# Performance work log

Measured on AMD Instinct MI355X. Metric: run time of the kernel, lower is better.

The kernel has to match this reference:

```python
import jax, jax.numpy as jnp
import numpy as np

C, E, H, TOPK = 768, 8, 3072, 2
B, T = 2048, 1

def setup_inputs() -> dict:
    key = jax.random.key(0)
    ks = jax.random.split(key, 5)
    proj_std = 0.02 * (2 * 12) ** (-0.5)  # n_layer = 12
    return {
        "x": jax.random.normal(ks[0], (B, T, C), jnp.float32),
        "w_router": 0.02 * jax.random.normal(ks[1], (C, E), jnp.float32),
        "w_c_fc": 0.02 * jax.random.normal(ks[2], (E, C, H), jnp.float32),
        "b_c_fc": jnp.zeros((E, 1, H), jnp.float32),
        "w_gate": 0.02 * jax.random.normal(ks[3], (E, C, H), jnp.float32),
        "b_gate": jnp.zeros((E, 1, H), jnp.float32),
        "w_c_proj": proj_std * jax.random.normal(ks[4], (E, H, C), jnp.float32),
        "b_c_proj": jnp.zeros((E, 1, C), jnp.float32),
        "top_k": TOPK,
    }

def reference(x, w_router, w_c_fc, b_c_fc, w_gate, b_gate, w_c_proj, b_c_proj, top_k):
    Bx, Tx, Cx = x.shape
    n_experts = w_c_fc.shape[0]
    xf = x.reshape(-1, Cx)                      # (N, C), N = B*T
    N = xf.shape[0]
    logits = xf @ w_router                      # (N, E); router has no bias (mlp_bias=False)
    top_k_logits, expert_indices = jax.lax.top_k(logits, top_k)   # (N, k)
    # put_along_axis into -inf, then softmax -> sparse routing probs
    sparse = jnp.full_like(logits, -jnp.inf)
    sparse = sparse.at[jnp.arange(N)[:, None], expert_indices].set(top_k_logits)
    expert_probs = jax.nn.softmax(sparse, axis=-1)                # (N, E)
    # dispatch: per-expert running position of each selected token
    mask = jax.nn.one_hot(expert_indices, n_experts, axis=-1).sum(axis=1)  # (N, E)
    positions = jnp.cumsum(mask, axis=0) * mask                   # (N, E)
    cap = top_k * Bx  # NOTE: module uses B (pre-flatten), not B*T
    ee, tt = jnp.nonzero(positions.T, size=cap)                   # expert id, token id
    pos = positions.T[ee, tt].astype(jnp.int32) - 1               # slot within expert buffer
    expert_inputs = jnp.zeros((n_experts, cap, Cx), x.dtype)
    expert_inputs = expert_inputs.at[ee, pos].set(xf[tt])         # (E, cap, C)
    # per-expert SwiGLU MLP (grouped GEMMs)
    h = jnp.einsum('eti,eih->eth', expert_inputs, w_c_fc) + b_c_fc
    g = jax.nn.silu(jnp.einsum('eti,eih->eth', expert_inputs, w_gate) + b_gate)
    o = jnp.einsum('eth,eho->eto', h * g, w_c_proj) + b_c_proj    # (E, cap, C)
    # combine: weighted scatter-add back to token order
    y = jnp.zeros_like(xf)
    y = y.at[tt].add(o[ee, pos] * expert_probs[tt, ee][:, None])  # (N, C)
    return y
```

## Files before the change

kernel.cpp:

```cpp
#include <hip/hip_runtime.h>
#include <hip/hip_bf16.h>
#include <cmath>

#define C_DIM 768
#define E_DIM 8
#define H_DIM 3072
#define CNT_STRIDE 32

typedef short s16x8 __attribute__((ext_vector_type(8)));
typedef short s16x4 __attribute__((ext_vector_type(4)));
typedef float f32x4 __attribute__((ext_vector_type(4)));

__device__ __forceinline__ float bf2f(unsigned short u) {
  unsigned int v = ((unsigned int)u) << 16;
  float f;
  __builtin_memcpy(&f, &v, 4);
  return f;
}

__device__ __forceinline__ unsigned short f2bf(float f) {
  __hip_bfloat16 h = __float2bfloat16(f);
  unsigned short u;
  __builtin_memcpy(&u, &h, 2);
  return u;
}

__global__ void cvt_kernel(const float* __restrict__ in, unsigned short* __restrict__ out, int n4) {
  int i = blockIdx.x * blockDim.x + threadIdx.x;
  const int stride = gridDim.x * blockDim.x;
  for (; i < n4; i += stride) {
    const float4 v = ((const float4*)in)[i];
    s16x4 p;
    p[0] = (short)f2bf(v.x);
    p[1] = (short)f2bf(v.y);
    p[2] = (short)f2bf(v.z);
    p[3] = (short)f2bf(v.w);
    *(s16x4*)(out + (size_t)i * 4) = p;
  }
}

__global__ void router_kernel(const float* __restrict__ x,
                              const float* __restrict__ w_r,
                              int* __restrict__ tok_e,
                              float* __restrict__ tok_p) {
  const int t = blockIdx.x;
  const int lane = threadIdx.x;
  float acc[E_DIM];
#pragma unroll
  for (int e = 0; e < E_DIM; ++e) acc[e] = 0.f;
  for (int c = lane; c < C_DIM; c += 64) {
    const float xv = x[(size_t)t * C_DIM + c];
    const float4 w0 = *(const float4*)(w_r + (size_t)c * E_DIM);
    const float4 w1 = *(const float4*)(w_r + (size_t)c * E_DIM + 4);
    acc[0] += xv * w0.x; acc[1] += xv * w0.y; acc[2] += xv * w0.z; acc[3] += xv * w0.w;
    acc[4] += xv * w1.x; acc[5] += xv * w1.y; acc[6] += xv * w1.z; acc[7] += xv * w1.w;
  }
#pragma unroll
  for (int e = 0; e < E_DIM; ++e) {
#pragma unroll
    for (int off = 32; off > 0; off >>= 1) acc[e] += __shfl_xor(acc[e], off, 64);
  }
  if (lane == 0) {
    int i0 = 0;
#pragma unroll
    for (int e = 1; e < E_DIM; ++e)
      if (acc[e] > acc[i0]) i0 = e;
    int i1 = (i0 == 0) ? 1 : 0;
#pragma unroll
    for (int e = 0; e < E_DIM; ++e)
      if (e != i0 && acc[e] > acc[i1]) i1 = e;
    const float d = expf(acc[i1] - acc[i0]);
    const float p0 = 1.f / (1.f + d);
    tok_e[2 * t] = i0;
    tok_e[2 * t + 1] = i1;
    tok_p[2 * t] = p0;
    tok_p[2 * t + 1] = 1.f - p0;
  }
}

__global__ void assign_kernel(const int* __restrict__ tok_e,
                              int* __restrict__ counts,
                              int* __restrict__ tok_rank,
                              int N) {
  __shared__ int lcnt[E_DIM];
  __shared__ int lbase[E_DIM];
  const int tid = threadIdx.x;
  const int t = blockIdx.x * blockDim.x + tid;
  if (tid < E_DIM) lcnt[tid] = 0;
  __syncthreads();
  int e0 = 0, e1 = 0, r0 = 0, r1 = 0;
  const bool valid = (t < N);
  if (valid) {
    e0 = tok_e[2 * t];
    e1 = tok_e[2 * t + 1];
    r0 = atomicAdd(&lcnt[e0], 1);
    r1 = atomicAdd(&lcnt[e1], 1);
  }
  __syncthreads();
  if (tid < E_DIM) lbase[tid] = atomicAdd(counts + tid * CNT_STRIDE, lcnt[tid]);
  __syncthreads();
  if (valid) {
    tok_rank[2 * t] = lbase[e0] + r0;
    tok_rank[2 * t + 1] = lbase[e1] + r1;
  }
}

__global__ void schedule_kernel(const int* __restrict__ counts,
                                int* __restrict__ pad_off,
                                int* __restrict__ table_e,
                                int* __restrict__ table_row,
                                int tableCap) {
  if (threadIdx.x != 0) return;
  int running = 0, idx = 0;
  for (int e = 0; e < E_DIM; ++e) {
    pad_off[e] = running;
    const int tiles = (counts[e * CNT_STRIDE] + 127) >> 7;
    for (int j = 0; j < tiles && idx < tableCap; ++j) {
      table_e[idx] = e;
      table_row[idx] = running + j * 128;
      ++idx;
    }
    running += tiles << 7;
  }
  for (; idx < tableCap; ++idx) table_e[idx] = -1;
}

__global__ void gather_kernel(const float* __restrict__ x,
                              const int* __restrict__ tok_e,
                              const int* __restrict__ tok_rank,
                              const int* __restrict__ pad_off,
                              int* __restrict__ tok_slot,
                              unsigned short* __restrict__ Xg) {
  const int t = blockIdx.x;
  const int lane = threadIdx.x;
  const int s0 = pad_off[tok_e[2 * t]] + tok_rank[2 * t];
  const int s1 = pad_off[tok_e[2 * t + 1]] + tok_rank[2 * t + 1];
  if (lane == 0) {
    tok_slot[2 * t] = s0;
    tok_slot[2 * t + 1] = s1;
  }
  const float4* src = (const float4*)(x + (size_t)t * C_DIM);
  for (int q = lane; q < C_DIM / 4; q += 64) {
    const float4 v = src[q];
    s16x4 p;
    p[0] = (short)f2bf(v.x);
    p[1] = (short)f2bf(v.y);
    p[2] = (short)f2bf(v.z);
    p[3] = (short)f2bf(v.w);
    *(s16x4*)(Xg + (size_t)s0 * C_DIM + q * 4) = p;
    *(s16x4*)(Xg + (size_t)s1 * C_DIM + q * 4) = p;
  }
}

__global__ __launch_bounds__(256, 2) void fcgate_kernel(
    const unsigned short* __restrict__ Xg, const unsigned short* __restrict__ w_fc,
    const float* __restrict__ b_fc, const unsigned short* __restrict__ w_gt,
    const float* __restrict__ b_gt, const int* __restrict__ table_e,
    const int* __restrict__ table_row, unsigned short* __restrict__ act) {
  const int mt = blockIdx.y;
  const int e = table_e[mt];
  if (e < 0) return;
  const int row0 = table_row[mt];
  const int nt = blockIdx.x;
  const int tid = threadIdx.x;
  const int lane = tid & 63;
  const int wid = tid >> 6;
  const int quad = lane >> 4;
  const int l16 = lane & 15;
  const int wrow = (wid >> 1) * 64;
  const int wcol = (wid & 1) * 32;

  __shared__ unsigned short As[128 * 40];
  __shared__ unsigned short Bs[2][32 * 72];

  const unsigned short* wptr[2];
  wptr[0] = w_fc + (size_t)e * C_DIM * H_DIM + nt * 64;
  wptr[1] = w_gt + (size_t)e * C_DIM * H_DIM + nt * 64;

  f32x4 accH[4][2], accG[4][2];
#pragma unroll
  for (int i = 0; i < 4; ++i)
#pragma unroll
    for (int j = 0; j < 2; ++j)
#pragma unroll
      for (int r = 0; r < 4; ++r) {
        accH[i][j][r] = 0.f;
        accG[i][j][r] = 0.f;
      }

  const int ar = tid >> 1;
  const int ac = (tid & 1) * 16;
  const int bk = tid >> 3;
  const int bn = (tid & 7) * 8;
  const int bcol = (bn + ((bk >> 3) << 4)) & 63;

  for (int k0 = 0; k0 < C_DIM; k0 += 32) {
    const uint4 av0 = *(const uint4*)(Xg + (size_t)(row0 + ar) * C_DIM + k0 + ac);
    const uint4 av1 = *(const uint4*)(Xg + (size_t)(row0 + ar) * C_DIM + k0 + ac + 8);
    const uint4 bv0 = *(const uint4*)(wptr[0] + (size_t)(k0 + bk) * H_DIM + bn);
    const uint4 bv1 = *(const uint4*)(wptr[1] + (size_t)(k0 + bk) * H_DIM + bn);
    __syncthreads();
    *(uint4*)(&As[ar * 40 + ac]) = av0;
    *(uint4*)(&As[ar * 40 + ac + 8]) = av1;
    *(uint4*)(&Bs[0][bk * 72 + bcol]) = bv0;
    *(uint4*)(&Bs[1][bk * 72 + bcol]) = bv1;
    __syncthreads();

    s16x8 afrag[4];
#pragma unroll
    for (int tr = 0; tr < 4; ++tr)
      afrag[tr] = *(const s16x8*)(&As[(wrow + tr * 16 + l16) * 40 + quad * 8]);

#pragma unroll
    for (int tc = 0; tc < 2; ++tc) {
      const int nn = wcol + tc * 16 + l16;
      const int ncol = (nn + (quad << 4)) & 63;
      s16x8 bF, bG;
#pragma unroll
      for (int j = 0; j < 8; ++j) {
        bF[j] = (short)Bs[0][(quad * 8 + j) * 72 + ncol];
        bG[j] = (short)Bs[1][(quad * 8 + j) * 72 + ncol];
      }
#pragma unroll
      for (int tr = 0; tr < 4; ++tr) {
        accH[tr][tc] = __builtin_amdgcn_mfma_f32_16x16x32_bf16(afrag[tr], bF, accH[tr][tc], 0, 0, 0);
        accG[tr][tc] = __builtin_amdgcn_mfma_f32_16x16x32_bf16(afrag[tr], bG, accG[tr][tc], 0, 0, 0);
      }
    }
  }

#pragma unroll
  for (int tc = 0; tc < 2; ++tc) {
    const int col = nt * 64 + wcol + tc * 16 + l16;
    const float bf = b_fc[e * H_DIM + col];
    const float bg = b_gt[e * H_DIM + col];
#pragma unroll
    for (int tr = 0; tr < 4; ++tr) {
#pragma unroll
      for (int r = 0; r < 4; ++r) {
        const int row = row0 + wrow + tr * 16 + quad * 4 + r;
        const float hv = accH[tr][tc][r] + bf;
        const float gv = accG[tr][tc][r] + bg;
        const float sv = gv / (1.f + __expf(-gv));
        act[(size_t)row * H_DIM + col] = f2bf(hv * sv);
      }
    }
  }
}

__global__ __launch_bounds__(256, 2) void proj_kernel(
    const unsigned short* __restrict__ act, const unsigned short* __restrict__ w_pj,
    const float* __restrict__ b_pj, const int* __restrict__ table_e,
    const int* __restrict__ table_row, float* __restrict__ o) {
  const int mt = blockIdx.y;
  const int e = table_e[mt];
  if (e < 0) return;
  const int row0 = table_row[mt];
  const int nt = blockIdx.x;
  const int tid = threadIdx.x;
  const int lane = tid & 63;
  const int wid = tid >> 6;
  const int quad = lane >> 4;
  const int l16 = lane & 15;
  const int wrow = (wid >> 1) * 64;
  const int wcol = (wid & 1) * 32;

  __shared__ unsigned short As[128 * 40];
  __shared__ unsigned short Bs[32 * 72];

  const unsigned short* wp = w_pj + (size_t)e * H_DIM * C_DIM + nt * 64;

  f32x4 acc[4][2];
#pragma unroll
  for (int i = 0; i < 4; ++i)
#pragma unroll
    for (int j = 0; j < 2; ++j)
#pragma unroll
      for (int r = 0; r < 4; ++r) acc[i][j][r] = 0.f;

  const int ar = tid >> 1;
  const int ac = (tid & 1) * 16;
  const int bk = tid >> 3;
  const int bn = (tid & 7) * 8;
  const int bcol = (bn + ((bk >> 3) << 4)) & 63;

  for (int k0 = 0; k0 < H_DIM; k0 += 32) {
    const uint4 av0 = *(const uint4*)(act + (size_t)(row0 + ar) * H_DIM + k0 + ac);
    const uint4 av1 = *(const uint4*)(act + (size_t)(row0 + ar) * H_DIM + k0 + ac + 8);
    const uint4 bv0 = *(const uint4*)(wp + (size_t)(k0 + bk) * C_DIM + bn);
    __syncthreads();
    *(uint4*)(&As[ar * 40 + ac]) = av0;
    *(uint4*)(&As[ar * 40 + ac + 8]) = av1;
    *(uint4*)(&Bs[bk * 72 + bcol]) = bv0;
    __syncthreads();

    s16x8 afrag[4];
#pragma unroll
    for (int tr = 0; tr < 4; ++tr)
      afrag[tr] = *(const s16x8*)(&As[(wrow + tr * 16 + l16) * 40 + quad * 8]);

#pragma unroll
    for (int tc = 0; tc < 2; ++tc) {
      const int nn = wcol + tc * 16 + l16;
      const int ncol = (nn + (quad << 4)) & 63;
      s16x8 bB;
#pragma unroll
      for (int j = 0; j < 8; ++j) bB[j] = (short)Bs[(quad * 8 + j) * 72 + ncol];
#pragma unroll
      for (int tr = 0; tr < 4; ++tr)
        acc[tr][tc] = __builtin_amdgcn_mfma_f32_16x16x32_bf16(afrag[tr], bB, acc[tr][tc], 0, 0, 0);
    }
  }

#pragma unroll
  for (int tc = 0; tc < 2; ++tc) {
    const int col = nt * 64 + wcol + tc * 16 + l16;
    const float bp = b_pj[e * C_DIM + col];
#pragma unroll
    for (int tr = 0; tr < 4; ++tr) {
#pragma unroll
      for (int r = 0; r < 4; ++r) {
        const int row = row0 + wrow + tr * 16 + quad * 4 + r;
        o[(size_t)row * C_DIM + col] = acc[tr][tc][r] + bp;
      }
    }
  }
}

__global__ void combine_kernel(const float* __restrict__ o,
                               const int* __restrict__ tok_slot,
                               const float* __restrict__ tok_p,
                               float* __restrict__ out) {
  const int t = blockIdx.x;
  const int lane = threadIdx.x;
  const int s0 = tok_slot[2 * t], s1 = tok_slot[2 * t + 1];
  const float p0 = tok_p[2 * t], p1 = tok_p[2 * t + 1];
  const f32x4* r0 = (const f32x4*)(o + (size_t)s0 * C_DIM);
  const f32x4* r1 = (const f32x4*)(o + (size_t)s1 * C_DIM);
  f32x4* dst = (f32x4*)(out + (size_t)t * C_DIM);
  for (int q = lane; q < C_DIM / 4; q += 64) {
    const f32x4 a = r0[q];
    const f32x4 b = r1[q];
    dst[q] = a * p0 + b * p1;
  }
}

extern "C" void kernel_launch(void* const* d_in, const int* in_sizes, int n_in,
                              void* d_out, int out_size, void* d_ws, size_t ws_size,
                              hipStream_t stream) {
  const int N = in_sizes[0] / C_DIM;
  char* ws = (char*)d_ws;

  int* counts = (int*)(ws + 0);
  int* pad_off = (int*)(ws + 1024);
  int* table_e = (int*)(ws + 1152);
  int* table_row = (int*)(ws + 1408);
  int* tok_e = (int*)(ws + 2048);
  float* tok_p = (float*)(ws + 2048 + (size_t)8 * N);
  int* tok_rank = (int*)(ws + 2048 + (size_t)16 * N);
  int* tok_slot = (int*)(ws + 2048 + (size_t)24 * N);

  int tableCap = (2 * N) / 128 + E_DIM;
  if (tableCap > 64) tableCap = 64;

  size_t off = 2048 + (size_t)32 * N;
  off = (off + 255) & ~(size_t)255;
  const size_t R = (size_t)2 * N + 128 * E_DIM;
  unsigned short* Xg = (unsigned short*)(ws + off);
  const size_t xg_bytes = R * C_DIM * 2;

  const size_t wbytes = (size_t)E_DIM * C_DIM * H_DIM * 2;
  size_t wfc_off = (off + xg_bytes + 255) & ~(size_t)255;
  size_t wgt_off = wfc_off + wbytes;
  size_t wpj_off = wgt_off + wbytes;
  unsigned short* wfc_bf = (unsigned short*)(ws + wfc_off);
  unsigned short* wgt_bf = (unsigned short*)(ws + wgt_off);
  unsigned short* wpj_bf = (unsigned short*)(ws + wpj_off);

  size_t act_off = (wpj_off + wbytes + 255) & ~(size_t)255;
  unsigned short* act = (unsigned short*)(ws + act_off);
  size_t o_off = (act_off + R * H_DIM * 2 + 255) & ~(size_t)255;
  float* o = (float*)(ws + o_off);
  const size_t need = o_off + R * C_DIM * 4;
  if (ws_size < need || n_in < 9) return;

  hipMemsetAsync(ws, 0, 2048, stream);
  hipMemsetAsync(Xg, 0, xg_bytes, stream);

  const int WN4 = (int)(E_DIM * C_DIM * H_DIM / 4);
  cvt_kernel<<<4096, 256, 0, stream>>>((const float*)d_in[2], wfc_bf, WN4);
  cvt_kernel<<<4096, 256, 0, stream>>>((const float*)d_in[4], wgt_bf, WN4);
  cvt_kernel<<<4096, 256, 0, stream>>>((const float*)d_in[6], wpj_bf, WN4);

  router_kernel<<<N, 64, 0, stream>>>((const float*)d_in[0], (const float*)d_in[1],
                                      tok_e, tok_p);
  assign_kernel<<<(N + 255) / 256, 256, 0, stream>>>(tok_e, counts, tok_rank, N);
  schedule_kernel<<<1, 64, 0, stream>>>(counts, pad_off, table_e, table_row, tableCap);
  gather_kernel<<<N, 64, 0, stream>>>((const float*)d_in[0], tok_e, tok_rank, pad_off,
                                      tok_slot, Xg);
  fcgate_kernel<<<dim3(H_DIM / 64, tableCap), 256, 0, stream>>>(
      Xg, wfc_bf, (const float*)d_in[3], wgt_bf, (const float*)d_in[5],
      table_e, table_row, act);
  proj_kernel<<<dim3(C_DIM / 64, tableCap), 256, 0, stream>>>(
      act, wpj_bf, (const float*)d_in[7], table_e, table_row, o);
  combine_kernel<<<N, 64, 0, stream>>>(o, tok_slot, tok_p, (float*)d_out);
}
```

Before: 421.6 us.

## Transpose weights to K-contiguous bf16 and widen fc/gate tile to 128 columns

```diff
diff --git a/kernel.cpp b/kernel.cpp
--- a/kernel.cpp
+++ b/kernel.cpp
@@ -25,18 +25,31 @@
   return u;
 }
 
-__global__ void cvt_kernel(const float* __restrict__ in, unsigned short* __restrict__ out, int n4) {
-  int i = blockIdx.x * blockDim.x + threadIdx.x;
-  const int stride = gridDim.x * blockDim.x;
-  for (; i < n4; i += stride) {
-    const float4 v = ((const float4*)in)[i];
-    s16x4 p;
-    p[0] = (short)f2bf(v.x);
-    p[1] = (short)f2bf(v.y);
-    p[2] = (short)f2bf(v.z);
-    p[3] = (short)f2bf(v.w);
-    *(s16x4*)(out + (size_t)i * 4) = p;
-  }
+__global__ void tr_cvt_kernel(const float* __restrict__ in, unsigned short* __restrict__ out,
+                              int R, int CC) {
+  const int e = blockIdx.z;
+  const int c0 = blockIdx.x * 64;
+  const int r0 = blockIdx.y * 64;
+  const int tid = threadIdx.x;
+  __shared__ unsigned short T[64 * 68];
+  const int row = tid >> 2;
+  const int cq = (tid & 3) * 4;
+  const float* src = in + (size_t)e * R * CC + (size_t)(r0 + row) * CC + c0;
+#pragma unroll
+  for (int j = 0; j < 4; ++j) {
+    const int c = cq + j * 16;
+    const float4 v = *(const float4*)(src + c);
+    T[(c + 0) * 68 + row] = f2bf(v.x);
+    T[(c + 1) * 68 + row] = f2bf(v.y);
+    T[(c + 2) * 68 + row] = f2bf(v.z);
+    T[(c + 3) * 68 + row] = f2bf(v.w);
+  }
+  __syncthreads();
+  const int oc = tid >> 2;
+  const int half = (tid & 3) * 16;
+  unsigned short* dst = out + (size_t)e * CC * R + (size_t)(c0 + oc) * R + r0 + half;
+  *(uint4*)(dst) = *(const uint4*)(&T[oc * 68 + half]);
+  *(uint4*)(dst + 8) = *(const uint4*)(&T[oc * 68 + half + 8]);
 }
 
 __global__ void router_kernel(const float* __restrict__ x,
@@ -153,8 +166,8 @@
 }
 
 __global__ __launch_bounds__(256, 2) void fcgate_kernel(
-    const unsigned short* __restrict__ Xg, const unsigned short* __restrict__ w_fc,
-    const float* __restrict__ b_fc, const unsigned short* __restrict__ w_gt,
+    const unsigned short* __restrict__ Xg, const unsigned short* __restrict__ wfcT,
+    const float* __restrict__ b_fc, const unsigned short* __restrict__ wgtT,
     const float* __restrict__ b_gt, const int* __restrict__ table_e,
     const int* __restrict__ table_row, unsigned short* __restrict__ act) {
   const int mt = blockIdx.y;
@@ -168,70 +181,68 @@
   const int quad = lane >> 4;
   const int l16 = lane & 15;
   const int wrow = (wid >> 1) * 64;
-  const int wcol = (wid & 1) * 32;
+  const int wcol = (wid & 1) * 64;
 
   __shared__ unsigned short As[128 * 40];
-  __shared__ unsigned short Bs[2][32 * 72];
-
-  const unsigned short* wptr[2];
-  wptr[0] = w_fc + (size_t)e * C_DIM * H_DIM + nt * 64;
-  wptr[1] = w_gt + (size_t)e * C_DIM * H_DIM + nt * 64;
-
-  f32x4 accH[4][2], accG[4][2];
+  __shared__ unsigned short BsF[128 * 40];
+  __shared__ unsigned short BsG[128 * 40];
+
+  const unsigned short* pF = wfcT + (size_t)e * H_DIM * C_DIM + (size_t)(nt * 128) * C_DIM;
+  const unsigned short* pG = wgtT + (size_t)e * H_DIM * C_DIM + (size_t)(nt * 128) * C_DIM;
+
+  f32x4 accH[4][4], accG[4][4];
 #pragma unroll
   for (int i = 0; i < 4; ++i)
 #pragma unroll
-    for (int j = 0; j < 2; ++j)
+    for (int j = 0; j < 4; ++j)
 #pragma unroll
       for (int r = 0; r < 4; ++r) {
         accH[i][j][r] = 0.f;
         accG[i][j][r] = 0.f;
       }
 
-  const int ar = tid >> 1;
-  const int ac = (tid & 1) * 16;
-  const int bk = tid >> 3;
-  const int bn = (tid & 7) * 8;
-  const int bcol = (bn + ((bk >> 3) << 4)) & 63;
+  const int sr = tid >> 1;
+  const int sc = (tid & 1) * 16;
 
   for (int k0 = 0; k0 < C_DIM; k0 += 32) {
-    const uint4 av0 = *(const uint4*)(Xg + (size_t)(row0 + ar) * C_DIM + k0 + ac);
-    const uint4 av1 = *(const uint4*)(Xg + (size_t)(row0 + ar) * C_DIM + k0 + ac + 8);
-    const uint4 bv0 = *(const uint4*)(wptr[0] + (size_t)(k0 + bk) * H_DIM + bn);
-    const uint4 bv1 = *(const uint4*)(wptr[1] + (size_t)(k0 + bk) * H_DIM + bn);
+    const uint4 av0 = *(const uint4*)(Xg + (size_t)(row0 + sr) * C_DIM + k0 + sc);
+    const uint4 av1 = *(const uint4*)(Xg + (size_t)(row0 + sr) * C_DIM + k0 + sc + 8);
+    const uint4 bf0 = *(const uint4*)(pF + (size_t)sr * C_DIM + k0 + sc);
+    const uint4 bf1 = *(const uint4*)(pF + (size_t)sr * C_DIM + k0 + sc + 8);
+    const uint4 bg0 = *(const uint4*)(pG + (size_t)sr * C_DIM + k0 + sc);
+    const uint4 bg1 = *(const uint4*)(pG + (size_t)sr * C_DIM + k0 + sc + 8);
     __syncthreads();
-    *(uint4*)(&As[ar * 40 + ac]) = av0;
-    *(uint4*)(&As[ar * 40 + ac + 8]) = av1;
-    *(uint4*)(&Bs[0][bk * 72 + bcol]) = bv0;
-    *(uint4*)(&Bs[1][bk * 72 + bcol]) = bv1;
+    *(uint4*)(&As[sr * 40 + sc]) = av0;
+    *(uint4*)(&As[sr * 40 + sc + 8]) = av1;
+    *(uint4*)(&BsF[sr * 40 + sc]) = bf0;
+    *(uint4*)(&BsF[sr * 40 + sc + 8]) = bf1;
+    *(uint4*)(&BsG[sr * 40 + sc]) = bg0;
+    *(uint4*)(&BsG[sr * 40 + sc + 8]) = bg1;
     __syncthreads();
 
-    s16x8 afrag[4];
+    s16x8 a[4], bF[4], bG[4];
 #pragma unroll
     for (int tr = 0; tr < 4; ++tr)
-      afrag[tr] = *(const s16x8*)(&As[(wrow + tr * 16 + l16) * 40 + quad * 8]);
-
-#pragma unroll
-    for (int tc = 0; tc < 2; ++tc) {
-      const int nn = wcol + tc * 16 + l16;
-      const int ncol = (nn + (quad << 4)) & 63;
-      s16x8 bF, bG;
-#pragma unroll
-      for (int j = 0; j < 8; ++j) {
-        bF[j] = (short)Bs[0][(quad * 8 + j) * 72 + ncol];
-        bG[j] = (short)Bs[1][(quad * 8 + j) * 72 + ncol];
+      a[tr] = *(const s16x8*)(&As[(wrow + tr * 16 + l16) * 40 + quad * 8]);
+#pragma unroll
+    for (int tc = 0; tc < 4; ++tc)
+      bF[tc] = *(const s16x8*)(&BsF[(wcol + tc * 16 + l16) * 40 + quad * 8]);
+#pragma unroll
+    for (int tc = 0; tc < 4; ++tc)
+      bG[tc] = *(const s16x8*)(&BsG[(wcol + tc * 16 + l16) * 40 + quad * 8]);
+
+#pragma unroll
+    for (int tr = 0; tr < 4; ++tr)
+#pragma unroll
+      for (int tc = 0; tc < 4; ++tc) {
+        accH[tr][tc] = __builtin_amdgcn_mfma_f32_16x16x32_bf16(a[tr], bF[tc], accH[tr][tc], 0, 0, 0);
+        accG[tr][tc] = __builtin_amdgcn_mfma_f32_16x16x32_bf16(a[tr], bG[tc], accG[tr][tc], 0, 0, 0);
       }
-#pragma unroll
-      for (int tr = 0; tr < 4; ++tr) {
-        accH[tr][tc] = __builtin_amdgcn_mfma_f32_16x16x32_bf16(afrag[tr], bF, accH[tr][tc], 0, 0, 0);
-        accG[tr][tc] = __builtin_amdgcn_mfma_f32_16x16x32_bf16(afrag[tr], bG, accG[tr][tc], 0, 0, 0);
-      }
-    }
-  }
-
-#pragma unroll
-  for (int tc = 0; tc < 2; ++tc) {
-    const int col = nt * 64 + wcol + tc * 16 + l16;
+  }
+
+#pragma unroll
+  for (int tc = 0; tc < 4; ++tc) {
+    const int col = nt * 128 + wcol + tc * 16 + l16;
     const float bf = b_fc[e * H_DIM + col];
     const float bg = b_gt[e * H_DIM + col];
 #pragma unroll
@@ -249,7 +260,7 @@
 }
 
 __global__ __launch_bounds__(256, 2) void proj_kernel(
-    const unsigned short* __restrict__ act, const unsigned short* __restrict__ w_pj,
+    const unsigned short* __restrict__ act, const unsigned short* __restrict__ wpjT,
     const float* __restrict__ b_pj, const int* __restrict__ table_e,
     const int* __restrict__ table_row, float* __restrict__ o) {
   const int mt = blockIdx.y;
@@ -266,9 +277,9 @@
   const int wcol = (wid & 1) * 32;
 
   __shared__ unsigned short As[128 * 40];
-  __shared__ unsigned short Bs[32 * 72];
-
-  const unsigned short* wp = w_pj + (size_t)e * H_DIM * C_DIM + nt * 64;
+  __shared__ unsigned short Bs[64 * 40];
+
+  const unsigned short* pB = wpjT + (size_t)e * C_DIM * H_DIM + (size_t)(nt * 64) * H_DIM;
 
   f32x4 acc[4][2];
 #pragma unroll
@@ -278,38 +289,34 @@
 #pragma unroll
       for (int r = 0; r < 4; ++r) acc[i][j][r] = 0.f;
 
-  const int ar = tid >> 1;
-  const int ac = (tid & 1) * 16;
-  const int bk = tid >> 3;
-  const int bn = (tid & 7) * 8;
-  const int bcol = (bn + ((bk >> 3) << 4)) & 63;
+  const int sr = tid >> 1;
+  const int sc = (tid & 1) * 16;
+  const int br = tid >> 2;
+  const int bc = (tid & 3) * 8;
 
   for (int k0 = 0; k0 < H_DIM; k0 += 32) {
-    const uint4 av0 = *(const uint4*)(act + (size_t)(row0 + ar) * H_DIM + k0 + ac);
-    const uint4 av1 = *(const uint4*)(act + (size_t)(row0 + ar) * H_DIM + k0 + ac + 8);
-    const uint4 bv0 = *(const uint4*)(wp + (size_t)(k0 + bk) * C_DIM + bn);
+    const uint4 av0 = *(const uint4*)(act + (size_t)(row0 + sr) * H_DIM + k0 + sc);
+    const uint4 av1 = *(const uint4*)(act + (size_t)(row0 + sr) * H_DIM + k0 + sc + 8);
+    const uint4 bv = *(const uint4*)(pB + (size_t)br * H_DIM + k0 + bc);
     __syncthreads();
-    *(uint4*)(&As[ar * 40 + ac]) = av0;
-    *(uint4*)(&As[ar * 40 + ac + 8]) = av1;
-    *(uint4*)(&Bs[bk * 72 + bcol]) = bv0;
+    *(uint4*)(&As[sr * 40 + sc]) = av0;
+    *(uint4*)(&As[sr * 40 + sc + 8]) = av1;
+    *(uint4*)(&Bs[br * 40 + bc]) = bv;
     __syncthreads();
 
-    s16x8 afrag[4];
+    s16x8 a[4], bB[2];
 #pragma unroll
     for (int tr = 0; tr < 4; ++tr)
-      afrag[tr] = *(const s16x8*)(&As[(wrow + tr * 16 + l16) * 40 + quad * 8]);
-
-#pragma unroll
-    for (int tc = 0; tc < 2; ++tc) {
-      const int nn = wcol + tc * 16 + l16;
-      const int ncol = (nn + (quad << 4)) & 63;
-      s16x8 bB;
-#pragma unroll
-      for (int j = 0; j < 8; ++j) bB[j] = (short)Bs[(quad * 8 + j) * 72 + ncol];
-#pragma unroll
-      for (int tr = 0; tr < 4; ++tr)
-        acc[tr][tc] = __builtin_amdgcn_mfma_f32_16x16x32_bf16(afrag[tr], bB, acc[tr][tc], 0, 0, 0);
-    }
+      a[tr] = *(const s16x8*)(&As[(wrow + tr * 16 + l16) * 40 + quad * 8]);
+#pragma unroll
+    for (int tc = 0; tc < 2; ++tc)
+      bB[tc] = *(const s16x8*)(&Bs[(wcol + tc * 16 + l16) * 40 + quad * 8]);
+
+#pragma unroll
+    for (int tr = 0; tr < 4; ++tr)
+#pragma unroll
+      for (int tc = 0; tc < 2; ++tc)
+        acc[tr][tc] = __builtin_amdgcn_mfma_f32_16x16x32_bf16(a[tr], bB[tc], acc[tr][tc], 0, 0, 0);
   }
 
 #pragma unroll
@@ -373,9 +380,9 @@
   size_t wfc_off = (off + xg_bytes + 255) & ~(size_t)255;
   size_t wgt_off = wfc_off + wbytes;
   size_t wpj_off = wgt_off + wbytes;
-  unsigned short* wfc_bf = (unsigned short*)(ws + wfc_off);
-  unsigned short* wgt_bf = (unsigned short*)(ws + wgt_off);
-  unsigned short* wpj_bf = (unsigned short*)(ws + wpj_off);
+  unsigned short* wfcT = (unsigned short*)(ws + wfc_off);
+  unsigned short* wgtT = (unsigned short*)(ws + wgt_off);
+  unsigned short* wpjT = (unsigned short*)(ws + wpj_off);
 
   size_t act_off = (wpj_off + wbytes + 255) & ~(size_t)255;
   unsigned short* act = (unsigned short*)(ws + act_off);
@@ -387,10 +394,12 @@
   hipMemsetAsync(ws, 0, 2048, stream);
   hipMemsetAsync(Xg, 0, xg_bytes, stream);
 
-  const int WN4 = (int)(E_DIM * C_DIM * H_DIM / 4);
-  cvt_kernel<<<4096, 256, 0, stream>>>((const float*)d_in[2], wfc_bf, WN4);
-  cvt_kernel<<<4096, 256, 0, stream>>>((const float*)d_in[4], wgt_bf, WN4);
-  cvt_kernel<<<4096, 256, 0, stream>>>((const float*)d_in[6], wpj_bf, WN4);
+  tr_cvt_kernel<<<dim3(H_DIM / 64, C_DIM / 64, E_DIM), 256, 0, stream>>>(
+      (const float*)d_in[2], wfcT, C_DIM, H_DIM);
+  tr_cvt_kernel<<<dim3(H_DIM / 64, C_DIM / 64, E_DIM), 256, 0, stream>>>(
+      (const float*)d_in[4], wgtT, C_DIM, H_DIM);
+  tr_cvt_kernel<<<dim3(C_DIM / 64, H_DIM / 64, E_DIM), 256, 0, stream>>>(
+      (const float*)d_in[6], wpjT, H_DIM, C_DIM);
 
   router_kernel<<<N, 64, 0, stream>>>((const float*)d_in[0], (const float*)d_in[1],
                                       tok_e, tok_p);
@@ -398,10 +407,10 @@
   schedule_kernel<<<1, 64, 0, stream>>>(counts, pad_off, table_e, table_row, tableCap);
   gather_kernel<<<N, 64, 0, stream>>>((const float*)d_in[0], tok_e, tok_rank, pad_off,
                                       tok_slot, Xg);
-  fcgate_kernel<<<dim3(H_DIM / 64, tableCap), 256, 0, stream>>>(
-      Xg, wfc_bf, (const float*)d_in[3], wgt_bf, (const float*)d_in[5],
+  fcgate_kernel<<<dim3(H_DIM / 128, tableCap), 256, 0, stream>>>(
+      Xg, wfcT, (const float*)d_in[3], wgtT, (const float*)d_in[5],
       table_e, table_row, act);
   proj_kernel<<<dim3(C_DIM / 64, tableCap), 256, 0, stream>>>(
-      act, wpj_bf, (const float*)d_in[7], table_e, table_row, o);
+      act, wpjT, (const float*)d_in[7], table_e, table_row, o);
   combine_kernel<<<N, 64, 0, stream>>>(o, tok_slot, tok_p, (float*)d_out);
 }
```

New measurement: 414.5 us. Within noise of the previous version (-1.7%).
